# Performance work log

Hardware: AMD Instinct MI355X
Metric: run time of the kernel (lower is better)

## Reference

```python
import math
import jax, jax.numpy as jnp
import numpy as np

B, S, D, ENC_D = 256, 110, 768, 128
H = 1
DH = D // H                      # 768 (single head)
MAXPOS = 110


def setup_inputs() -> dict:
    key = jax.random.key(0)
    ks = jax.random.split(key, 16)
    w = lambda k, shape: (jax.random.normal(k, shape, jnp.float32) * 0.02)
    return {
        "im_repr": jax.random.normal(ks[0], (B, ENC_D), jnp.float32),
        "q_repr": jax.random.normal(ks[1], (B, S, D), jnp.float32),
        # self-attention (QFAttentionMH, is_cross_attention=False)
        "mha_wq": w(ks[2], (D, D)), "mha_bq": jnp.zeros((D,), jnp.float32),
        "mha_wk": w(ks[3], (D, D)), "mha_bk": jnp.zeros((D,), jnp.float32),
        "mha_wv": w(ks[4], (D, D)), "mha_bv": jnp.zeros((D,), jnp.float32),
        "mha_de": w(ks[5], (2 * MAXPOS - 1, DH)),
        # cross-attention (encoder_hidden_size=128)
        "ca_wq": w(ks[6], (D, D)), "ca_bq": jnp.zeros((D,), jnp.float32),
        "ca_wk": w(ks[7], (ENC_D, D)), "ca_bk": jnp.zeros((D,), jnp.float32),
        "ca_wv": w(ks[8], (ENC_D, D)), "ca_bv": jnp.zeros((D,), jnp.float32),
        "ca_de": w(ks[9], (2 * MAXPOS - 1, DH)),
        # QFIntermediate: 768 -> 256 -> 768, LayerNorm(768)
        "fi_w1": w(ks[10], (D, 256)), "fi_b1": jnp.zeros((256,), jnp.float32),
        "fi_w2": w(ks[11], (256, D)), "fi_b2": jnp.zeros((D,), jnp.float32),
        "ln_g": jnp.ones((D,), jnp.float32), "ln_b": jnp.zeros((D,), jnp.float32),
    }


def _attention(hs, kv, wq, bq, wk, bk, wv, bv):
    # hs: [B, Sq, D] queries; kv: [B, Sk, Dk] key/value source
    b, sq, _ = hs.shape
    sk = kv.shape[1]
    q = (hs @ wq + bq).reshape(b, sq, H, DH).transpose(0, 2, 1, 3)   # [b,h,sq,dh]
    k = (kv @ wk + bk).reshape(b, sk, H, DH).transpose(0, 2, 1, 3)
    v = (kv @ wv + bv).reshape(b, sk, H, DH).transpose(0, 2, 1, 3)
    # NOTE (faithful to source): the torch module computes a relative-position
    # bias (distance_embedding gather + einsum) and adds it to attention_scores,
    # but then immediately OVERWRITES attention_scores with a fresh QK^T matmul,
    # so the bias has NO effect on the output. We replicate the effective math.
    scores = jnp.einsum('bhqd,bhkd->bhqk', q, k) / math.sqrt(DH)
    probs = jax.nn.softmax(scores, axis=-1)
    # dropout is identity in eval mode
    ctx = jnp.einsum('bhqk,bhkd->bhqd', probs, v)
    return ctx.transpose(0, 2, 1, 3).reshape(b, sq, D)


def reference(im_repr, q_repr,
              mha_wq, mha_bq, mha_wk, mha_bk, mha_wv, mha_bv, mha_de,
              ca_wq, ca_bq, ca_wk, ca_bk, ca_wv, ca_bv, ca_de,
              fi_w1, fi_b1, fi_w2, fi_b2, ln_g, ln_b):
    # self-attention over text queries
    q_attn = _attention(q_repr, q_repr, mha_wq, mha_bq, mha_wk, mha_bk, mha_wv, mha_bv)
    # vision repr broadcast to the query seq length, used as K/V source
    b, s = q_repr.shape[0], q_repr.shape[1]
    vis = jnp.broadcast_to(im_repr[:, None, :], (b, s, im_repr.shape[-1]))
    x = _attention(q_attn, vis, ca_wq, ca_bq, ca_wk, ca_bk, ca_wv, ca_bv).mean(axis=1)  # [B, D]
    # QFIntermediate: dense -> GELU -> dense -> (dropout=id) -> LN(residual)
    h = jax.nn.gelu(x @ fi_w1 + fi_b1, approximate=False)   # torch nn.GELU default = exact
    h = h @ fi_w2 + fi_b2
    y = x + h
    mu = jnp.mean(y, axis=-1, keepdims=True)
    var = jnp.var(y, axis=-1, keepdims=True)
    out = (y - mu) / jnp.sqrt(var + 1e-12) * ln_g + ln_b
    return out
```

## Files before the change

kernel.cpp:

```cpp
#include <hip/hip_runtime.h>
#include <math.h>


#define DMODEL 768
#define ENCD   128
#define HID    256
#define KC     4
#define KW     192

#define WS_X   0
#define WS_P   196608
#define WS_W2Q 458752

__device__ __forceinline__ float gelu_exact(float v) {
    return 0.5f * v * (1.f + erff(v * 0.70710678118654752f));
}
__device__ __forceinline__ unsigned short f2bf(float f) {
    unsigned u = __float_as_uint(f);
    u = (u + 0x7FFFu + ((u >> 16) & 1u)) >> 16;
    return (unsigned short)u;
}
__device__ __forceinline__ float bflo(unsigned u) { return __uint_as_float(u << 16); }
__device__ __forceinline__ float bfhi(unsigned u) { return __uint_as_float(u & 0xFFFF0000u); }
__device__ __forceinline__ unsigned packbf(float a, float b) {
    return (unsigned)f2bf(a) | ((unsigned)f2bf(b) << 16);
}

__global__ __launch_bounds__(512) void kA(
    const float* __restrict__ im,
    const float* __restrict__ wv,
    const float* __restrict__ bv,
    const float* __restrict__ w1,
    const float* __restrict__ w2,
    float* __restrict__ ws)
{
    __shared__ float im_s[4][ENCD];
    __shared__ float xp[2][4][KW];
    __shared__ float x_s[4][KW];
    __shared__ float php[2][4][HID];
    const int t  = threadIdx.x;
    const int kc = blockIdx.x;
    const int r0 = blockIdx.y * 4;

    if (t < 96) {
        const int qid = (blockIdx.y * KC + kc) * 96 + t;
        const int k8 = qid / DMODEL, col = qid % DMODEL;
        const float* src = w2 + (8 * k8) * DMODEL + col;
        uint4 u;
        u.x = packbf(src[0],          src[DMODEL]);
        u.y = packbf(src[2 * DMODEL], src[3 * DMODEL]);
        u.z = packbf(src[4 * DMODEL], src[5 * DMODEL]);
        u.w = packbf(src[6 * DMODEL], src[7 * DMODEL]);
        ((uint4*)(ws + WS_W2Q))[qid] = u;
    }

    im_s[t >> 7][t & 127] = im[(r0 + (t >> 7)) * ENCD + (t & 127)];
    __syncthreads();

    if (t < 2 * KW) {
        const int col = t % KW, eh = t / KW;
        const int colg = kc * KW + col;
        float a0 = 0.f, a1 = 0.f, a2 = 0.f, a3 = 0.f;
        const int e0 = eh * (ENCD / 2);
        #pragma unroll 16
        for (int e = e0; e < e0 + ENCD / 2; ++e) {
            float w = wv[e * DMODEL + colg];
            a0 += im_s[0][e] * w;
            a1 += im_s[1][e] * w;
            a2 += im_s[2][e] * w;
            a3 += im_s[3][e] * w;
        }
        xp[eh][0][col] = a0;
        xp[eh][1][col] = a1;
        xp[eh][2][col] = a2;
        xp[eh][3][col] = a3;
    }
    __syncthreads();
    if (t < KW) {
        const int colg = kc * KW + t;
        const float b = bv[colg];
        #pragma unroll
        for (int r = 0; r < 4; ++r) {
            float v = xp[0][r][t] + xp[1][r][t] + b;
            ws[WS_X + (r0 + r) * DMODEL + colg] = v;
            x_s[r][t] = v;
        }
    }
    __syncthreads();

    {
        const int j = t & 255, kh = t >> 8;
        const int kbase = kh * (KW / 2);
        float c0 = 0.f, c1 = 0.f, c2 = 0.f, c3 = 0.f;
        const float* w1c = w1 + (kc * KW + kbase) * HID;
        #pragma unroll 16
        for (int k = 0; k < KW / 2; ++k) {
            float w = w1c[k * HID + j];
            c0 += x_s[0][kbase + k] * w;
            c1 += x_s[1][kbase + k] * w;
            c2 += x_s[2][kbase + k] * w;
            c3 += x_s[3][kbase + k] * w;
        }
        php[kh][0][j] = c0;
        php[kh][1][j] = c1;
        php[kh][2][j] = c2;
        php[kh][3][j] = c3;
    }
    __syncthreads();
    if (t < HID) {
        float* p = ws + WS_P + kc * (256 * HID);
        #pragma unroll
        for (int r = 0; r < 4; ++r)
            p[(r0 + r) * HID + t] = php[0][r][t] + php[1][r][t];
    }
}

__global__ __launch_bounds__(768) void kB(
    const float* __restrict__ b1,
    const float* __restrict__ b2,
    const float* __restrict__ gam,
    const float* __restrict__ bet,
    const float* __restrict__ ws,
    float* __restrict__ out)
{
    __shared__ float h_s[HID];
    __shared__ float red[12][2];
    const int t = threadIdx.x, r = blockIdx.x;

    if (t < HID) {
        const float* p = ws + WS_P;
        float v = b1[t];
        #pragma unroll
        for (int kc = 0; kc < KC; ++kc)
            v += p[kc * (256 * HID) + r * HID + t];
        h_s[t] = gelu_exact(v);
    }
    __syncthreads();

    const uint4* w2q = (const uint4*)(ws + WS_W2Q);
    float a0 = 0.f, a1 = 0.f, a2 = 0.f, a3 = 0.f;
    #pragma unroll 4
    for (int k8 = 0; k8 < 32; ++k8) {
        uint4 u = w2q[k8 * DMODEL + t];
        const int j = 8 * k8;
        a0 += h_s[j + 0] * bflo(u.x); a1 += h_s[j + 1] * bfhi(u.x);
        a2 += h_s[j + 2] * bflo(u.y); a3 += h_s[j + 3] * bfhi(u.y);
        a0 += h_s[j + 4] * bflo(u.z); a1 += h_s[j + 5] * bfhi(u.z);
        a2 += h_s[j + 6] * bflo(u.w); a3 += h_s[j + 7] * bfhi(u.w);
    }
    const float y = ws[WS_X + r * DMODEL + t] + b2[t] + ((a0 + a1) + (a2 + a3));

    float s = y, q = y * y;
    #pragma unroll
    for (int off = 32; off > 0; off >>= 1) {
        s += __shfl_down(s, off);
        q += __shfl_down(q, off);
    }
    const int lane = t & 63, wave = t >> 6;
    if (lane == 0) { red[wave][0] = s; red[wave][1] = q; }
    __syncthreads();

    float ss = 0.f, qq = 0.f;
    #pragma unroll
    for (int w = 0; w < 12; ++w) { ss += red[w][0]; qq += red[w][1]; }
    const float mu   = ss * (1.f / DMODEL);
    const float rstd = rsqrtf(qq * (1.f / DMODEL) - mu * mu + 1e-12f);

    out[r * DMODEL + t] = (y - mu) * rstd * gam[t] + bet[t];
}

extern "C" void kernel_launch(void* const* d_in, const int* in_sizes, int n_in,
                              void* d_out, int out_size, void* d_ws, size_t ws_size,
                              hipStream_t stream) {
    const float* im  = (const float*)d_in[0];
    const float* wv  = (const float*)d_in[13];
    const float* bv  = (const float*)d_in[14];
    const float* w1  = (const float*)d_in[16];
    const float* b1  = (const float*)d_in[17];
    const float* w2  = (const float*)d_in[18];
    const float* b2  = (const float*)d_in[19];
    const float* g   = (const float*)d_in[20];
    const float* bt  = (const float*)d_in[21];
    float* out = (float*)d_out;
    float* ws  = (float*)d_ws;

    kA<<<dim3(KC, 64), 512, 0, stream>>>(im, wv, bv, w1, w2, ws);
    kB<<<dim3(256),    768, 0, stream>>>(b1, b2, g, bt, ws, out);
}
```

Measured before the change: 20.43 us.

## Vectorize GEMV loops with float4, split K further, and prefetch W2 in kB

kA's two GEMV phases now load weights as float4 per thread and split the reduction dimension across 8 slices instead of 2, summing the partials in shared memory. This spreads the weight reads over more threads with wider loads and shortens each thread's serial loop. The W2 bf16 packing now runs in its own threads alongside the first GEMV rather than before it. kB issues the first eight W2 loads plus the residual and bias loads before the barrier, so their latency overlaps the GELU phase, at the cost of more registers and shared memory.

Measured after the change: 17.80 us (median of 2 runs). 12.9% less time.

```diff
diff --git a/kernel.cpp b/kernel.cpp
--- a/kernel.cpp
+++ b/kernel.cpp
@@ -35,15 +35,37 @@
     float* __restrict__ ws)
 {
     __shared__ float im_s[4][ENCD];
-    __shared__ float xp[2][4][KW];
+    __shared__ float xp[8][4][KW];
     __shared__ float x_s[4][KW];
-    __shared__ float php[2][4][HID];
+    __shared__ float php[8][4][HID];
     const int t  = threadIdx.x;
     const int kc = blockIdx.x;
     const int r0 = blockIdx.y * 4;
 
-    if (t < 96) {
-        const int qid = (blockIdx.y * KC + kc) * 96 + t;
+    im_s[t >> 7][t & 127] = im[(r0 + (t >> 7)) * ENCD + (t & 127)];
+    __syncthreads();
+
+    if (t < 384) {
+        const int q = t % 48, s = t / 48;
+        const int colg = kc * KW + 4 * q;
+        const int e0 = s * 16;
+        float4 a0 = {0,0,0,0}, a1 = {0,0,0,0}, a2 = {0,0,0,0}, a3 = {0,0,0,0};
+        #pragma unroll 8
+        for (int e = e0; e < e0 + 16; ++e) {
+            const float4 w = *(const float4*)(wv + e * DMODEL + colg);
+            const float i0 = im_s[0][e], i1 = im_s[1][e];
+            const float i2 = im_s[2][e], i3 = im_s[3][e];
+            a0.x += i0 * w.x; a0.y += i0 * w.y; a0.z += i0 * w.z; a0.w += i0 * w.w;
+            a1.x += i1 * w.x; a1.y += i1 * w.y; a1.z += i1 * w.z; a1.w += i1 * w.w;
+            a2.x += i2 * w.x; a2.y += i2 * w.y; a2.z += i2 * w.z; a2.w += i2 * w.w;
+            a3.x += i3 * w.x; a3.y += i3 * w.y; a3.z += i3 * w.z; a3.w += i3 * w.w;
+        }
+        ((float4*)xp[s][0])[q] = a0;
+        ((float4*)xp[s][1])[q] = a1;
+        ((float4*)xp[s][2])[q] = a2;
+        ((float4*)xp[s][3])[q] = a3;
+    } else if (t < 480) {
+        const int qid = (blockIdx.y * KC + kc) * 96 + (t - 384);
         const int k8 = qid / DMODEL, col = qid % DMODEL;
         const float* src = w2 + (8 * k8) * DMODEL + col;
         uint4 u;
@@ -53,35 +75,16 @@
         u.w = packbf(src[6 * DMODEL], src[7 * DMODEL]);
         ((uint4*)(ws + WS_W2Q))[qid] = u;
     }
-
-    im_s[t >> 7][t & 127] = im[(r0 + (t >> 7)) * ENCD + (t & 127)];
-    __syncthreads();
-
-    if (t < 2 * KW) {
-        const int col = t % KW, eh = t / KW;
-        const int colg = kc * KW + col;
-        float a0 = 0.f, a1 = 0.f, a2 = 0.f, a3 = 0.f;
-        const int e0 = eh * (ENCD / 2);
-        #pragma unroll 16
-        for (int e = e0; e < e0 + ENCD / 2; ++e) {
-            float w = wv[e * DMODEL + colg];
-            a0 += im_s[0][e] * w;
-            a1 += im_s[1][e] * w;
-            a2 += im_s[2][e] * w;
-            a3 += im_s[3][e] * w;
-        }
-        xp[eh][0][col] = a0;
-        xp[eh][1][col] = a1;
-        xp[eh][2][col] = a2;
-        xp[eh][3][col] = a3;
-    }
-    __syncthreads();
+    __syncthreads();
+
     if (t < KW) {
         const int colg = kc * KW + t;
         const float b = bv[colg];
         #pragma unroll
         for (int r = 0; r < 4; ++r) {
-            float v = xp[0][r][t] + xp[1][r][t] + b;
+            float v = b;
+            #pragma unroll
+            for (int s = 0; s < 8; ++s) v += xp[s][r][t];
             ws[WS_X + (r0 + r) * DMODEL + colg] = v;
             x_s[r][t] = v;
         }
@@ -89,29 +92,37 @@
     __syncthreads();
 
     {
-        const int j = t & 255, kh = t >> 8;
-        const int kbase = kh * (KW / 2);
-        float c0 = 0.f, c1 = 0.f, c2 = 0.f, c3 = 0.f;
-        const float* w1c = w1 + (kc * KW + kbase) * HID;
-        #pragma unroll 16
-        for (int k = 0; k < KW / 2; ++k) {
-            float w = w1c[k * HID + j];
-            c0 += x_s[0][kbase + k] * w;
-            c1 += x_s[1][kbase + k] * w;
-            c2 += x_s[2][kbase + k] * w;
-            c3 += x_s[3][kbase + k] * w;
-        }
-        php[kh][0][j] = c0;
-        php[kh][1][j] = c1;
-        php[kh][2][j] = c2;
-        php[kh][3][j] = c3;
-    }
-    __syncthreads();
+        const int jq = t & 63, ks = t >> 6;
+        const int k0 = ks * 24;
+        float4 a0 = {0,0,0,0}, a1 = {0,0,0,0}, a2 = {0,0,0,0}, a3 = {0,0,0,0};
+        const float* w1c = w1 + (size_t)kc * KW * HID;
+        #pragma unroll 8
+        for (int kk = 0; kk < 24; ++kk) {
+            const int k = k0 + kk;
+            const float4 w = *(const float4*)(w1c + k * HID + 4 * jq);
+            const float x0 = x_s[0][k], x1 = x_s[1][k];
+            const float x2 = x_s[2][k], x3 = x_s[3][k];
+            a0.x += x0 * w.x; a0.y += x0 * w.y; a0.z += x0 * w.z; a0.w += x0 * w.w;
+            a1.x += x1 * w.x; a1.y += x1 * w.y; a1.z += x1 * w.z; a1.w += x1 * w.w;
+            a2.x += x2 * w.x; a2.y += x2 * w.y; a2.z += x2 * w.z; a2.w += x2 * w.w;
+            a3.x += x3 * w.x; a3.y += x3 * w.y; a3.z += x3 * w.z; a3.w += x3 * w.w;
+        }
+        ((float4*)php[ks][0])[jq] = a0;
+        ((float4*)php[ks][1])[jq] = a1;
+        ((float4*)php[ks][2])[jq] = a2;
+        ((float4*)php[ks][3])[jq] = a3;
+    }
+    __syncthreads();
+
     if (t < HID) {
         float* p = ws + WS_P + kc * (256 * HID);
         #pragma unroll
-        for (int r = 0; r < 4; ++r)
-            p[(r0 + r) * HID + t] = php[0][r][t] + php[1][r][t];
+        for (int r = 0; r < 4; ++r) {
+            float v = 0.f;
+            #pragma unroll
+            for (int s = 0; s < 8; ++s) v += php[s][r][t];
+            p[(r0 + r) * HID + t] = v;
+        }
     }
 }
 
@@ -127,6 +138,18 @@
     __shared__ float red[12][2];
     const int t = threadIdx.x, r = blockIdx.x;
 
+    const uint4* w2q = (const uint4*)(ws + WS_W2Q);
+    uint4 u0 = w2q[0 * DMODEL + t];
+    uint4 u1 = w2q[1 * DMODEL + t];
+    uint4 u2 = w2q[2 * DMODEL + t];
+    uint4 u3 = w2q[3 * DMODEL + t];
+    uint4 u4 = w2q[4 * DMODEL + t];
+    uint4 u5 = w2q[5 * DMODEL + t];
+    uint4 u6 = w2q[6 * DMODEL + t];
+    uint4 u7 = w2q[7 * DMODEL + t];
+    const float xv  = ws[WS_X + r * DMODEL + t];
+    const float b2v = b2[t];
+
     if (t < HID) {
         const float* p = ws + WS_P;
         float v = b1[t];
@@ -137,18 +160,22 @@
     }
     __syncthreads();
 
-    const uint4* w2q = (const uint4*)(ws + WS_W2Q);
     float a0 = 0.f, a1 = 0.f, a2 = 0.f, a3 = 0.f;
+    #define PROC(U, J)                                                  \
+        a0 += h_s[(J) + 0] * bflo(U.x); a1 += h_s[(J) + 1] * bfhi(U.x); \
+        a2 += h_s[(J) + 2] * bflo(U.y); a3 += h_s[(J) + 3] * bfhi(U.y); \
+        a0 += h_s[(J) + 4] * bflo(U.z); a1 += h_s[(J) + 5] * bfhi(U.z); \
+        a2 += h_s[(J) + 6] * bflo(U.w); a3 += h_s[(J) + 7] * bfhi(U.w);
+    PROC(u0, 0)  PROC(u1, 8)  PROC(u2, 16) PROC(u3, 24)
+    PROC(u4, 32) PROC(u5, 40) PROC(u6, 48) PROC(u7, 56)
     #pragma unroll 4
-    for (int k8 = 0; k8 < 32; ++k8) {
+    for (int k8 = 8; k8 < 32; ++k8) {
         uint4 u = w2q[k8 * DMODEL + t];
         const int j = 8 * k8;
-        a0 += h_s[j + 0] * bflo(u.x); a1 += h_s[j + 1] * bfhi(u.x);
-        a2 += h_s[j + 2] * bflo(u.y); a3 += h_s[j + 3] * bfhi(u.y);
-        a0 += h_s[j + 4] * bflo(u.z); a1 += h_s[j + 5] * bfhi(u.z);
-        a2 += h_s[j + 6] * bflo(u.w); a3 += h_s[j + 7] * bfhi(u.w);
-    }
-    const float y = ws[WS_X + r * DMODEL + t] + b2[t] + ((a0 + a1) + (a2 + a3));
+        PROC(u, j)
+    }
+    #undef PROC
+    const float y = xv + b2v + ((a0 + a1) + (a2 + a3));
 
     float s = y, q = y * y;
     #pragma unroll
```
